# Kernel optimization log

Measured on AMD Instinct MI355X. Metric: run time of the kernel, lower is better.

The kernel has to match this reference:

```python
import jax, jax.numpy as jnp
import numpy as np

N, E = 100000, 1600000
IN_C, H, C = 256, 4, 64
NEG_SLOPE = 0.2


def setup_inputs() -> dict:
    key = jax.random.key(0)
    k1, k2, k3, k4, k5 = jax.random.split(key, 5)
    x = jax.random.normal(k1, (N, IN_C), dtype=jnp.float32)
    edge_index = jax.random.randint(k2, (2, E), 0, N, dtype=jnp.int64)
    # GATConv params: lin weight [IN_C, H*C], attention vectors [H, C], bias [C] (concat=False)
    W = jax.random.normal(k3, (IN_C, H * C), dtype=jnp.float32) / np.sqrt(IN_C)
    att_src = jax.random.normal(k4, (H, C), dtype=jnp.float32) / np.sqrt(C)
    att_dst = jax.random.normal(k5, (H, C), dtype=jnp.float32) / np.sqrt(C)
    bias = jnp.zeros((C,), dtype=jnp.float32)
    return {"x": x, "edge_index": edge_index, "W": W,
            "att_src": att_src, "att_dst": att_dst, "bias": bias}


def reference(x, edge_index, W, att_src, att_dst, bias):
    n = x.shape[0]
    # GATConv adds self-loops by default
    loops = jnp.arange(n, dtype=edge_index.dtype)
    src = jnp.concatenate([edge_index[0], loops])  # message source j
    dst = jnp.concatenate([edge_index[1], loops])  # message target i

    h = (x @ W).reshape(n, H, C)                       # [N,H,C]
    a_src = jnp.einsum('nhc,hc->nh', h, att_src)       # [N,H]
    a_dst = jnp.einsum('nhc,hc->nh', h, att_dst)       # [N,H]

    e = jax.nn.leaky_relu(a_src[src] + a_dst[dst], NEG_SLOPE)  # [E+N,H]
    m = jax.ops.segment_max(e, dst, num_segments=n)            # per-target max
    e = jnp.exp(e - m[dst])
    denom = jax.ops.segment_sum(e, dst, num_segments=n)
    alpha = e / (denom[dst] + 1e-16)                           # softmax over incoming edges

    out = jax.ops.segment_sum(alpha[:, :, None] * h[src], dst, num_segments=n)  # [N,H,C]
    return out.mean(axis=1) + bias  # concat=False -> mean over heads, [N,C]
```

## Files before the change

kernel.cpp:

```cpp
#include <hip/hip_runtime.h>

#define N_NODES 100000
#define N_EDGES 1600000
#define TOT (N_EDGES + N_NODES)
#define IN_CH 256
#define NHEAD 4
#define CH 64
#define HC 256
#define NEG_SLOPE 0.2f

typedef _Float16 half8 __attribute__((ext_vector_type(8)));
typedef _Float16 h2v __attribute__((ext_vector_type(2)));
typedef float f32x4 __attribute__((ext_vector_type(4)));
typedef unsigned short ushort_t;
typedef unsigned int uint_t;

static __device__ __forceinline__ ushort_t f2h(float f) {
  _Float16 h = (_Float16)f;
  return __builtin_bit_cast(ushort_t, h);
}

__global__ __launch_bounds__(256) void conv_w(const float* __restrict__ W,
                                              ushort_t* __restrict__ Wt) {
  int n = blockIdx.x * 4 + (threadIdx.x >> 6);
  int k0 = (threadIdx.x & 63) * 4;
  ushort4 u;
  u.x = f2h(W[(size_t)(k0 + 0) * HC + n]);
  u.y = f2h(W[(size_t)(k0 + 1) * HC + n]);
  u.z = f2h(W[(size_t)(k0 + 2) * HC + n]);
  u.w = f2h(W[(size_t)(k0 + 3) * HC + n]);
  *reinterpret_cast<ushort4*>(&Wt[(size_t)n * IN_CH + k0]) = u;
}

#define GBM 128
#define GBK 32
#define LDA 40

__global__ __launch_bounds__(256) void gemm_mfma(const float* __restrict__ X,
                                                 const ushort_t* __restrict__ Wt,
                                                 const float* __restrict__ att_src,
                                                 const float* __restrict__ att_dst,
                                                 uint2* __restrict__ Hmp,
                                                 float* __restrict__ as_out,
                                                 float* __restrict__ ad_out,
                                                 const int* __restrict__ edst,
                                                 int* __restrict__ deg, int M) {
  __shared__ __align__(16) ushort_t As[GBM][LDA];
  __shared__ __align__(16) ushort_t Bs[HC][LDA];
  const int tid = threadIdx.x;
  const int lane = tid & 63;
  const int wid = tid >> 6;
  const int l16 = lane & 15;
  const int lhi = lane >> 4;
  const int row0 = blockIdx.x * GBM;

  f32x4 acc[2][16] = {};

  for (int k0 = 0; k0 < IN_CH; k0 += GBK) {
    {
      int r = tid >> 1;
      int c0 = (tid & 1) * 16;
      int gr = row0 + r;
      float4 v0, v1, v2, v3;
      if (gr < M) {
        const float4* p = reinterpret_cast<const float4*>(X + (size_t)gr * IN_CH + k0 + c0);
        v0 = p[0]; v1 = p[1]; v2 = p[2]; v3 = p[3];
      } else {
        v0 = v1 = v2 = v3 = make_float4(0.f, 0.f, 0.f, 0.f);
      }
      uint4 u0, u1;
      u0.x = __builtin_bit_cast(uint_t, __builtin_amdgcn_cvt_pkrtz(v0.x, v0.y));
      u0.y = __builtin_bit_cast(uint_t, __builtin_amdgcn_cvt_pkrtz(v0.z, v0.w));
      u0.z = __builtin_bit_cast(uint_t, __builtin_amdgcn_cvt_pkrtz(v1.x, v1.y));
      u0.w = __builtin_bit_cast(uint_t, __builtin_amdgcn_cvt_pkrtz(v1.z, v1.w));
      u1.x = __builtin_bit_cast(uint_t, __builtin_amdgcn_cvt_pkrtz(v2.x, v2.y));
      u1.y = __builtin_bit_cast(uint_t, __builtin_amdgcn_cvt_pkrtz(v2.z, v2.w));
      u1.z = __builtin_bit_cast(uint_t, __builtin_amdgcn_cvt_pkrtz(v3.x, v3.y));
      u1.w = __builtin_bit_cast(uint_t, __builtin_amdgcn_cvt_pkrtz(v3.z, v3.w));
      *reinterpret_cast<uint4*>(&As[r][c0]) = u0;
      *reinterpret_cast<uint4*>(&As[r][c0 + 8]) = u1;
    }
    {
      const uint4* p = reinterpret_cast<const uint4*>(Wt + (size_t)tid * IN_CH + k0);
      uint4 w0 = p[0], w1 = p[1];
      *reinterpret_cast<uint4*>(&Bs[tid][0]) = w0;
      *reinterpret_cast<uint4*>(&Bs[tid][8]) = w1;
      p = reinterpret_cast<const uint4*>(Wt + (size_t)tid * IN_CH + k0 + 16);
      uint4 w2 = p[0], w3 = p[1];
      *reinterpret_cast<uint4*>(&Bs[tid][16]) = w2;
      *reinterpret_cast<uint4*>(&Bs[tid][24]) = w3;
    }
    __syncthreads();
    half8 a0 = *reinterpret_cast<const half8*>(&As[wid * 32 + l16][lhi * 8]);
    half8 a1 = *reinterpret_cast<const half8*>(&As[wid * 32 + 16 + l16][lhi * 8]);
#pragma unroll
    for (int n = 0; n < 16; ++n) {
      half8 b = *reinterpret_cast<const half8*>(&Bs[n * 16 + l16][lhi * 8]);
      acc[0][n] = __builtin_amdgcn_mfma_f32_16x16x32_f16(a0, b, acc[0][n], 0, 0, 0);
      acc[1][n] = __builtin_amdgcn_mfma_f32_16x16x32_f16(a1, b, acc[1][n], 0, 0, 0);
    }
    __syncthreads();
  }

  float attS[16], attD[16];
#pragma unroll
  for (int n = 0; n < 16; ++n) {
    attS[n] = att_src[n * 16 + l16];
    attD[n] = att_dst[n * 16 + l16];
  }

#pragma unroll
  for (int m = 0; m < 2; ++m) {
#pragma unroll
    for (int r = 0; r < 4; ++r) {
      int grow = row0 + wid * 32 + m * 16 + lhi * 4 + r;
      if (grow < M) {
#pragma unroll
        for (int n2 = 0; n2 < 4; ++n2) {
          uint_t pk01 = __builtin_bit_cast(uint_t,
              __builtin_amdgcn_cvt_pkrtz(acc[m][n2][r], acc[m][n2 + 4][r]));
          uint_t pk23 = __builtin_bit_cast(uint_t,
              __builtin_amdgcn_cvt_pkrtz(acc[m][n2 + 8][r], acc[m][n2 + 12][r]));
          Hmp[(size_t)grow * 64 + n2 * 16 + l16] = make_uint2(pk01, pk23);
        }
        float s[4] = {0.f, 0.f, 0.f, 0.f}, d[4] = {0.f, 0.f, 0.f, 0.f};
#pragma unroll
        for (int h = 0; h < 4; ++h)
#pragma unroll
          for (int j = 0; j < 4; ++j) {
            s[h] += acc[m][h * 4 + j][r] * attS[h * 4 + j];
            d[h] += acc[m][h * 4 + j][r] * attD[h * 4 + j];
          }
#pragma unroll
        for (int off = 1; off < 16; off <<= 1)
#pragma unroll
          for (int h = 0; h < 4; ++h) {
            s[h] += __shfl_xor(s[h], off, 16);
            d[h] += __shfl_xor(d[h], off, 16);
          }
        if (l16 == 0) {
#pragma unroll
          for (int h = 0; h < 4; ++h) {
            as_out[(size_t)grow * 4 + h] = s[h];
            ad_out[(size_t)grow * 4 + h] = d[h];
          }
        }
      }
    }
  }

#pragma unroll
  for (int i = 0; i < 2; ++i) {
    int t = blockIdx.x * 512 + i * 256 + tid;
    if (t < N_EDGES / 4) {
      int4 d4 = reinterpret_cast<const int4*>(edst)[t];
      atomicAdd(&deg[d4.x], 1);
      atomicAdd(&deg[d4.y], 1);
      atomicAdd(&deg[d4.z], 1);
      atomicAdd(&deg[d4.w], 1);
    }
  }
}

__global__ __launch_bounds__(256) void scan1(const int* __restrict__ deg,
                                             int* __restrict__ rp,
                                             int* __restrict__ bsum) {
  __shared__ int sh[256];
  int t = threadIdx.x;
  int base = blockIdx.x * 1024 + t * 4;
  int v[4];
#pragma unroll
  for (int i = 0; i < 4; ++i) v[i] = (base + i < N_NODES) ? (deg[base + i] + 1) : 0;
  int tsum = v[0] + v[1] + v[2] + v[3];
  sh[t] = tsum;
  __syncthreads();
  for (int off = 1; off < 256; off <<= 1) {
    int x = (t >= off) ? sh[t - off] : 0;
    __syncthreads();
    sh[t] += x;
    __syncthreads();
  }
  if (t == 255) bsum[blockIdx.x] = sh[255];
  int run = sh[t] - tsum;
#pragma unroll
  for (int i = 0; i < 4; ++i) {
    if (base + i < N_NODES) rp[base + i] = run;
    run += v[i];
  }
}

#define NBLK1 ((N_NODES + 1023) / 1024)

__global__ __launch_bounds__(128) void scan2(const int* __restrict__ bsum,
                                             int* __restrict__ boff) {
  __shared__ int sh[128];
  int t = threadIdx.x;
  int own = (t < NBLK1) ? bsum[t] : 0;
  sh[t] = own;
  __syncthreads();
  for (int off = 1; off < 128; off <<= 1) {
    int x = (t >= off) ? sh[t - off] : 0;
    __syncthreads();
    sh[t] += x;
    __syncthreads();
  }
  boff[t] = sh[t] - own;
}

__global__ __launch_bounds__(256) void scan3(int* __restrict__ rp,
                                             const int* __restrict__ boff,
                                             int* __restrict__ cursor) {
  int idx = blockIdx.x * 256 + threadIdx.x;
  if (idx < N_NODES) {
    int v = rp[idx] + boff[idx >> 10];
    rp[idx] = v;
    cursor[idx] = v;
  }
  if (idx == 0) rp[N_NODES] = TOT;
}

__global__ __launch_bounds__(256) void scatter_edges(const int* __restrict__ esrc,
                                                     const int* __restrict__ edst,
                                                     const float* __restrict__ as_buf,
                                                     const float* __restrict__ ad_buf,
                                                     int* __restrict__ cursor,
                                                     uint4* __restrict__ erec) {
  int e = blockIdx.x * 256 + threadIdx.x;
  if (e >= TOT) return;
  int s, d;
  if (e < N_EDGES) { s = esrc[e]; d = edst[e]; }
  else { s = e - N_EDGES; d = s; }
  int p = atomicAdd(&cursor[d], 1);
  float4 a1 = *reinterpret_cast<const float4*>(as_buf + (size_t)s * NHEAD);
  float4 a2 = *reinterpret_cast<const float4*>(ad_buf + (size_t)d * NHEAD);
  float e0 = a1.x + a2.x; e0 = e0 > 0.f ? e0 : NEG_SLOPE * e0;
  float e1 = a1.y + a2.y; e1 = e1 > 0.f ? e1 : NEG_SLOPE * e1;
  float e2 = a1.z + a2.z; e2 = e2 > 0.f ? e2 : NEG_SLOPE * e2;
  float e3 = a1.w + a2.w; e3 = e3 > 0.f ? e3 : NEG_SLOPE * e3;
  float w0 = __expf(e0 - 4.f), w1 = __expf(e1 - 4.f);
  float w2 = __expf(e2 - 4.f), w3 = __expf(e3 - 4.f);
  uint_t pk01 = __builtin_bit_cast(uint_t, __builtin_amdgcn_cvt_pkrtz(w0, w1));
  uint_t pk23 = __builtin_bit_cast(uint_t, __builtin_amdgcn_cvt_pkrtz(w2, w3));
  erec[p] = make_uint4((uint_t)s, pk01, pk23, 0u);
}

__global__ __launch_bounds__(256) void aggregate(const int* __restrict__ rp,
                                                 const uint4* __restrict__ erec,
                                                 const uint2* __restrict__ Hp,
                                                 const float* __restrict__ bias,
                                                 float* __restrict__ out) {
  int n = blockIdx.x * 4 + (threadIdx.x >> 6);
  int lane = threadIdx.x & 63;
  if (n >= N_NODES) return;
  const int half = lane >> 5;
  const uint_t off_lane = (uint_t)(lane & 31) << 4;
  const char* __restrict__ Hb = (const char*)Hp;

  int beg = rp[n], end = rp[n + 1];
  const int last = end - 1;

  float acc[8] = {};
  float den[4] = {};

  int ia = beg + half;     if (ia > last) ia = last;
  int ib = beg + 2 + half; if (ib > last) ib = last;
  uint4 rec_a = erec[ia];
  uint4 rec_b = erec[ib];

  for (int j = beg; j < end; j += 4) {
    uint4 cur_a = rec_a;
    uint4 cur_b = rec_b;
    ia = j + 4 + half; if (ia > last) ia = last;
    ib = j + 6 + half; if (ib > last) ib = last;
    rec_a = erec[ia];
    rec_b = erec[ib];

    uint_t hoff_a = (cur_a.x << 9) | off_lane;
    uint_t hoff_b = (cur_b.x << 9) | off_lane;
    uint4 hva = *reinterpret_cast<const uint4*>(Hb + hoff_a);
    uint4 hvb = *reinterpret_cast<const uint4*>(Hb + hoff_b);

    bool act_a = (j + half) < end;
    bool act_b = (j + 2 + half) < end;
    uint_t wa01u = act_a ? cur_a.y : 0u;
    uint_t wa23u = act_a ? cur_a.z : 0u;
    uint_t wb01u = act_b ? cur_b.y : 0u;
    uint_t wb23u = act_b ? cur_b.z : 0u;

    h2v wa01 = __builtin_bit_cast(h2v, wa01u);
    h2v wa23 = __builtin_bit_cast(h2v, wa23u);
    h2v wb01 = __builtin_bit_cast(h2v, wb01u);
    h2v wb23 = __builtin_bit_cast(h2v, wb23u);

    h2v haa = __builtin_bit_cast(h2v, hva.x);
    h2v hab = __builtin_bit_cast(h2v, hva.y);
    h2v hac = __builtin_bit_cast(h2v, hva.z);
    h2v had = __builtin_bit_cast(h2v, hva.w);

    acc[0] += (float)wa01.x * (float)haa.x;
    acc[1] += (float)wa01.y * (float)haa.y;
    acc[2] += (float)wa23.x * (float)hab.x;
    acc[3] += (float)wa23.y * (float)hab.y;
    acc[4] += (float)wa01.x * (float)hac.x;
    acc[5] += (float)wa01.y * (float)hac.y;
    acc[6] += (float)wa23.x * (float)had.x;
    acc[7] += (float)wa23.y * (float)had.y;
    den[0] += (float)wa01.x;
    den[1] += (float)wa01.y;
    den[2] += (float)wa23.x;
    den[3] += (float)wa23.y;

    h2v hba = __builtin_bit_cast(h2v, hvb.x);
    h2v hbb = __builtin_bit_cast(h2v, hvb.y);
    h2v hbc = __builtin_bit_cast(h2v, hvb.z);
    h2v hbd = __builtin_bit_cast(h2v, hvb.w);

    acc[0] += (float)wb01.x * (float)hba.x;
    acc[1] += (float)wb01.y * (float)hba.y;
    acc[2] += (float)wb23.x * (float)hbb.x;
    acc[3] += (float)wb23.y * (float)hbb.y;
    acc[4] += (float)wb01.x * (float)hbc.x;
    acc[5] += (float)wb01.y * (float)hbc.y;
    acc[6] += (float)wb23.x * (float)hbd.x;
    acc[7] += (float)wb23.y * (float)hbd.y;
    den[0] += (float)wb01.x;
    den[1] += (float)wb01.y;
    den[2] += (float)wb23.x;
    den[3] += (float)wb23.y;
  }

#pragma unroll
  for (int k = 0; k < 8; ++k) acc[k] += __shfl_xor(acc[k], 32, 64);
#pragma unroll
  for (int k = 0; k < 4; ++k) den[k] += __shfl_xor(den[k], 32, 64);

  if (lane < 32) {
    float i0 = 1.f / (den[0] + 1e-30f);
    float i1 = 1.f / (den[1] + 1e-30f);
    float i2 = 1.f / (den[2] + 1e-30f);
    float i3 = 1.f / (den[3] + 1e-30f);
    float2 b2 = *reinterpret_cast<const float2*>(bias + 2 * lane);
    float rA = 0.25f * (acc[0] * i0 + acc[1] * i1 + acc[2] * i2 + acc[3] * i3) + b2.x;
    float rB = 0.25f * (acc[4] * i0 + acc[5] * i1 + acc[6] * i2 + acc[7] * i3) + b2.y;
    *reinterpret_cast<float2*>(out + (size_t)n * CH + 2 * lane) = make_float2(rA, rB);
  }
}

extern "C" void kernel_launch(void* const* d_in, const int* in_sizes, int n_in,
                              void* d_out, int out_size, void* d_ws, size_t ws_size,
                              hipStream_t stream) {
  const float* x       = (const float*)d_in[0];
  const int*   eidx    = (const int*)d_in[1];
  const float* W       = (const float*)d_in[2];
  const float* att_src = (const float*)d_in[3];
  const float* att_dst = (const float*)d_in[4];
  const float* bias    = (const float*)d_in[5];
  float* out = (float*)d_out;

  uint2*    Hmp    = (uint2*)d_ws;
  uint4*    erec   = (uint4*)(Hmp + (size_t)N_NODES * 64);
  float*    as_buf = (float*)(erec + (size_t)TOT);
  float*    ad_buf = as_buf + (size_t)N_NODES * NHEAD;
  ushort_t* Wt     = (ushort_t*)(ad_buf + (size_t)N_NODES * NHEAD);
  int*      deg    = (int*)(Wt + 65536);
  int*      rp     = deg + N_NODES;
  int*      bsum   = rp + N_NODES + 1;
  int*      boff   = bsum + 128;

  const int* esrc = eidx;
  const int* edst = eidx + N_EDGES;

  conv_w<<<64, 256, 0, stream>>>(W, Wt);
  hipMemsetAsync(deg, 0, (size_t)N_NODES * sizeof(int), stream);

  dim3 ggrid((N_NODES + GBM - 1) / GBM);
  gemm_mfma<<<ggrid, 256, 0, stream>>>(x, Wt, att_src, att_dst, Hmp, as_buf, ad_buf,
                                       edst, deg, N_NODES);

  scan1<<<NBLK1, 256, 0, stream>>>(deg, rp, bsum);
  scan2<<<1, 128, 0, stream>>>(bsum, boff);
  scan3<<<(N_NODES + 255) / 256, 256, 0, stream>>>(rp, boff, deg );
  scatter_edges<<<(TOT + 255) / 256, 256, 0, stream>>>(esrc, edst, as_buf, ad_buf,
                                                       deg , erec);

  aggregate<<<(N_NODES + 3) / 4, 256, 0, stream>>>(rp, erec, Hmp, bias, out);
}
```

Measured before the change: 338.4 us.

## Drop LDS staging in GEMM, load MFMA operands from global, split degree count

The projection GEMM no longer stages X and W tiles through shared memory with barriers. Each wave now loads its 16-row A fragment and the fp16 W fragments straight from global memory (W is small and should stay cached), with 64 rows per block and a launch bound requesting higher occupancy. The degree-counting atomics move out of the GEMM into a separate count_deg kernel. This removes LDS traffic and syncs, at the cost of redundant W reads from L2 per wave, halved register tiling per wave, and an extra kernel launch.

```diff
diff --git a/kernel.cpp b/kernel.cpp
--- a/kernel.cpp
+++ b/kernel.cpp
@@ -32,74 +32,44 @@
   *reinterpret_cast<ushort4*>(&Wt[(size_t)n * IN_CH + k0]) = u;
 }
 
-#define GBM 128
-#define GBK 32
-#define LDA 40
-
-__global__ __launch_bounds__(256) void gemm_mfma(const float* __restrict__ X,
-                                                 const ushort_t* __restrict__ Wt,
-                                                 const float* __restrict__ att_src,
-                                                 const float* __restrict__ att_dst,
-                                                 uint2* __restrict__ Hmp,
-                                                 float* __restrict__ as_out,
-                                                 float* __restrict__ ad_out,
-                                                 const int* __restrict__ edst,
-                                                 int* __restrict__ deg, int M) {
-  __shared__ __align__(16) ushort_t As[GBM][LDA];
-  __shared__ __align__(16) ushort_t Bs[HC][LDA];
+#define GROWS 64
+
+__global__ __launch_bounds__(256, 4) void gemm_mfma(const float* __restrict__ X,
+                                                    const ushort_t* __restrict__ Wt,
+                                                    const float* __restrict__ att_src,
+                                                    const float* __restrict__ att_dst,
+                                                    uint2* __restrict__ Hmp,
+                                                    float* __restrict__ as_out,
+                                                    float* __restrict__ ad_out, int M) {
   const int tid = threadIdx.x;
   const int lane = tid & 63;
   const int wid = tid >> 6;
   const int l16 = lane & 15;
   const int lhi = lane >> 4;
-  const int row0 = blockIdx.x * GBM;
-
-  f32x4 acc[2][16] = {};
-
-  for (int k0 = 0; k0 < IN_CH; k0 += GBK) {
-    {
-      int r = tid >> 1;
-      int c0 = (tid & 1) * 16;
-      int gr = row0 + r;
-      float4 v0, v1, v2, v3;
-      if (gr < M) {
-        const float4* p = reinterpret_cast<const float4*>(X + (size_t)gr * IN_CH + k0 + c0);
-        v0 = p[0]; v1 = p[1]; v2 = p[2]; v3 = p[3];
-      } else {
-        v0 = v1 = v2 = v3 = make_float4(0.f, 0.f, 0.f, 0.f);
-      }
-      uint4 u0, u1;
-      u0.x = __builtin_bit_cast(uint_t, __builtin_amdgcn_cvt_pkrtz(v0.x, v0.y));
-      u0.y = __builtin_bit_cast(uint_t, __builtin_amdgcn_cvt_pkrtz(v0.z, v0.w));
-      u0.z = __builtin_bit_cast(uint_t, __builtin_amdgcn_cvt_pkrtz(v1.x, v1.y));
-      u0.w = __builtin_bit_cast(uint_t, __builtin_amdgcn_cvt_pkrtz(v1.z, v1.w));
-      u1.x = __builtin_bit_cast(uint_t, __builtin_amdgcn_cvt_pkrtz(v2.x, v2.y));
-      u1.y = __builtin_bit_cast(uint_t, __builtin_amdgcn_cvt_pkrtz(v2.z, v2.w));
-      u1.z = __builtin_bit_cast(uint_t, __builtin_amdgcn_cvt_pkrtz(v3.x, v3.y));
-      u1.w = __builtin_bit_cast(uint_t, __builtin_amdgcn_cvt_pkrtz(v3.z, v3.w));
-      *reinterpret_cast<uint4*>(&As[r][c0]) = u0;
-      *reinterpret_cast<uint4*>(&As[r][c0 + 8]) = u1;
+  const int row0 = blockIdx.x * GROWS;
+
+  int rowA = row0 + wid * 16 + l16;
+  int rowA_c = rowA < M ? rowA : M - 1;
+  const float* __restrict__ xrow = X + (size_t)rowA_c * IN_CH + lhi * 8;
+  const ushort_t* __restrict__ wbase = Wt + (size_t)l16 * IN_CH + lhi * 8;
+
+  f32x4 acc[16] = {};
+
+#pragma unroll 2
+  for (int k0 = 0; k0 < IN_CH; k0 += 32) {
+    float4 xa = *reinterpret_cast<const float4*>(xrow + k0);
+    float4 xb = *reinterpret_cast<const float4*>(xrow + k0 + 4);
+    uint4 ua;
+    ua.x = __builtin_bit_cast(uint_t, __builtin_amdgcn_cvt_pkrtz(xa.x, xa.y));
+    ua.y = __builtin_bit_cast(uint_t, __builtin_amdgcn_cvt_pkrtz(xa.z, xa.w));
+    ua.z = __builtin_bit_cast(uint_t, __builtin_amdgcn_cvt_pkrtz(xb.x, xb.y));
+    ua.w = __builtin_bit_cast(uint_t, __builtin_amdgcn_cvt_pkrtz(xb.z, xb.w));
+    half8 a = __builtin_bit_cast(half8, ua);
+#pragma unroll
+    for (int n = 0; n < 16; ++n) {
+      half8 b = *reinterpret_cast<const half8*>(wbase + (size_t)n * 16 * IN_CH + k0);
+      acc[n] = __builtin_amdgcn_mfma_f32_16x16x32_f16(a, b, acc[n], 0, 0, 0);
     }
-    {
-      const uint4* p = reinterpret_cast<const uint4*>(Wt + (size_t)tid * IN_CH + k0);
-      uint4 w0 = p[0], w1 = p[1];
-      *reinterpret_cast<uint4*>(&Bs[tid][0]) = w0;
-      *reinterpret_cast<uint4*>(&Bs[tid][8]) = w1;
-      p = reinterpret_cast<const uint4*>(Wt + (size_t)tid * IN_CH + k0 + 16);
-      uint4 w2 = p[0], w3 = p[1];
-      *reinterpret_cast<uint4*>(&Bs[tid][16]) = w2;
-      *reinterpret_cast<uint4*>(&Bs[tid][24]) = w3;
-    }
-    __syncthreads();
-    half8 a0 = *reinterpret_cast<const half8*>(&As[wid * 32 + l16][lhi * 8]);
-    half8 a1 = *reinterpret_cast<const half8*>(&As[wid * 32 + 16 + l16][lhi * 8]);
-#pragma unroll
-    for (int n = 0; n < 16; ++n) {
-      half8 b = *reinterpret_cast<const half8*>(&Bs[n * 16 + l16][lhi * 8]);
-      acc[0][n] = __builtin_amdgcn_mfma_f32_16x16x32_f16(a0, b, acc[0][n], 0, 0, 0);
-      acc[1][n] = __builtin_amdgcn_mfma_f32_16x16x32_f16(a1, b, acc[1][n], 0, 0, 0);
-    }
-    __syncthreads();
   }
 
   float attS[16], attD[16];
@@ -110,56 +80,52 @@
   }
 
 #pragma unroll
-  for (int m = 0; m < 2; ++m) {
-#pragma unroll
-    for (int r = 0; r < 4; ++r) {
-      int grow = row0 + wid * 32 + m * 16 + lhi * 4 + r;
-      if (grow < M) {
-#pragma unroll
-        for (int n2 = 0; n2 < 4; ++n2) {
-          uint_t pk01 = __builtin_bit_cast(uint_t,
-              __builtin_amdgcn_cvt_pkrtz(acc[m][n2][r], acc[m][n2 + 4][r]));
-          uint_t pk23 = __builtin_bit_cast(uint_t,
-              __builtin_amdgcn_cvt_pkrtz(acc[m][n2 + 8][r], acc[m][n2 + 12][r]));
-          Hmp[(size_t)grow * 64 + n2 * 16 + l16] = make_uint2(pk01, pk23);
+  for (int r = 0; r < 4; ++r) {
+    int grow = row0 + wid * 16 + lhi * 4 + r;
+    if (grow < M) {
+#pragma unroll
+      for (int n2 = 0; n2 < 4; ++n2) {
+        uint_t pk01 = __builtin_bit_cast(uint_t,
+            __builtin_amdgcn_cvt_pkrtz(acc[n2][r], acc[n2 + 4][r]));
+        uint_t pk23 = __builtin_bit_cast(uint_t,
+            __builtin_amdgcn_cvt_pkrtz(acc[n2 + 8][r], acc[n2 + 12][r]));
+        Hmp[(size_t)grow * 64 + n2 * 16 + l16] = make_uint2(pk01, pk23);
+      }
+      float s[4] = {0.f, 0.f, 0.f, 0.f}, d[4] = {0.f, 0.f, 0.f, 0.f};
+#pragma unroll
+      for (int h = 0; h < 4; ++h)
+#pragma unroll
+        for (int j = 0; j < 4; ++j) {
+          s[h] += acc[h * 4 + j][r] * attS[h * 4 + j];
+          d[h] += acc[h * 4 + j][r] * attD[h * 4 + j];
         }
-        float s[4] = {0.f, 0.f, 0.f, 0.f}, d[4] = {0.f, 0.f, 0.f, 0.f};
-#pragma unroll
-        for (int h = 0; h < 4; ++h)
-#pragma unroll
-          for (int j = 0; j < 4; ++j) {
-            s[h] += acc[m][h * 4 + j][r] * attS[h * 4 + j];
-            d[h] += acc[m][h * 4 + j][r] * attD[h * 4 + j];
-          }
-#pragma unroll
-        for (int off = 1; off < 16; off <<= 1)
-#pragma unroll
-          for (int h = 0; h < 4; ++h) {
-            s[h] += __shfl_xor(s[h], off, 16);
-            d[h] += __shfl_xor(d[h], off, 16);
-          }
-        if (l16 == 0) {
-#pragma unroll
-          for (int h = 0; h < 4; ++h) {
-            as_out[(size_t)grow * 4 + h] = s[h];
-            ad_out[(size_t)grow * 4 + h] = d[h];
-          }
+#pragma unroll
+      for (int off = 1; off < 16; off <<= 1)
+#pragma unroll
+        for (int h = 0; h < 4; ++h) {
+          s[h] += __shfl_xor(s[h], off, 16);
+          d[h] += __shfl_xor(d[h], off, 16);
+        }
+      if (l16 == 0) {
+#pragma unroll
+        for (int h = 0; h < 4; ++h) {
+          as_out[(size_t)grow * 4 + h] = s[h];
+          ad_out[(size_t)grow * 4 + h] = d[h];
         }
       }
     }
   }
-
-#pragma unroll
-  for (int i = 0; i < 2; ++i) {
-    int t = blockIdx.x * 512 + i * 256 + tid;
-    if (t < N_EDGES / 4) {
-      int4 d4 = reinterpret_cast<const int4*>(edst)[t];
-      atomicAdd(&deg[d4.x], 1);
-      atomicAdd(&deg[d4.y], 1);
-      atomicAdd(&deg[d4.z], 1);
-      atomicAdd(&deg[d4.w], 1);
-    }
-  }
+}
+
+__global__ __launch_bounds__(256) void count_deg(const int* __restrict__ edst,
+                                                 int* __restrict__ deg) {
+  int t = blockIdx.x * 256 + threadIdx.x;
+  if (t >= N_EDGES / 4) return;
+  int4 d4 = reinterpret_cast<const int4*>(edst)[t];
+  atomicAdd(&deg[d4.x], 1);
+  atomicAdd(&deg[d4.y], 1);
+  atomicAdd(&deg[d4.z], 1);
+  atomicAdd(&deg[d4.w], 1);
 }
 
 __global__ __launch_bounds__(256) void scan1(const int* __restrict__ deg,
@@ -372,10 +338,10 @@
 
   conv_w<<<64, 256, 0, stream>>>(W, Wt);
   hipMemsetAsync(deg, 0, (size_t)N_NODES * sizeof(int), stream);
-
-  dim3 ggrid((N_NODES + GBM - 1) / GBM);
-  gemm_mfma<<<ggrid, 256, 0, stream>>>(x, Wt, att_src, att_dst, Hmp, as_buf, ad_buf,
-                                       edst, deg, N_NODES);
+  count_deg<<<(N_EDGES / 4 + 255) / 256, 256, 0, stream>>>(edst, deg);
+
+  dim3 ggrid((N_NODES + GROWS - 1) / GROWS);
+  gemm_mfma<<<ggrid, 256, 0, stream>>>(x, Wt, att_src, att_dst, Hmp, as_buf, ad_buf, N_NODES);
 
   scan1<<<NBLK1, 256, 0, stream>>>(deg, rp, bsum);
   scan2<<<1, 128, 0, stream>>>(bsum, boff);
```

Result: slower. 394.1 us (+16.5%).
